# Optimization experiments

Measured on AMD Instinct MI355X. Metric: run time of the kernel, lower is better.

Reference implementation:

```python
import jax, jax.numpy as jnp
import numpy as np

MUL = 32          # multiplicity of 0e and 1o channels
NRAD = 8          # radial basis size
NPATH = 7         # TP instructions

# Orthonormal symmetric-traceless basis for the real l=2 irrep -> Cartesian map
_B = np.zeros((5, 3, 3))
_s2 = 1.0 / np.sqrt(2.0)
_B[0, 0, 1] = _B[0, 1, 0] = _s2                      # xy
_B[1, 1, 2] = _B[1, 2, 1] = _s2                      # yz
_B[2] = np.diag([-1.0, -1.0, 2.0]) / np.sqrt(6.0)    # 2z^2-x^2-y^2
_B[3, 0, 2] = _B[3, 2, 0] = _s2                      # xz
_B[4] = np.diag([1.0, -1.0, 0.0]) / np.sqrt(2.0)     # x^2-y^2
# w3j(1,2,1)[i,M,k], Frobenius-normalized to 1 (e3nn convention)
C121 = jnp.asarray(np.transpose(_B, (1, 0, 2)) / np.sqrt(5.0), jnp.float32)
INV_SQRT3 = float(1.0 / np.sqrt(3.0))   # w3j(1,1,0) / w3j(0,1,1) / w3j(1,0,1)
A0 = float(1.0 / np.sqrt(64.0))         # path weight, l=0 outs: sqrt(1/fan_in), fan_in=2*32
A1 = float(np.sqrt(3.0 / 96.0))         # path weight, l=1 out: sqrt((2l+1)/fan_in), fan_in=3*32


def setup_inputs() -> dict:
    key = jax.random.key(0)
    ks = jax.random.split(key, 9)
    N, E = 4096, 32768
    x = jax.random.normal(ks[0], (N, 4 * MUL), jnp.float32)
    edge_attr = jax.random.normal(ks[1], (E, 9), jnp.float32)
    edge_length = jax.random.uniform(ks[2], (E,), jnp.float32) * 5.0
    edge_src = jax.random.randint(ks[3], (E,), 0, N)
    edge_dst = jax.random.randint(ks[4], (E,), 0, N)
    W_fc1 = jax.random.normal(ks[5], (NRAD, 64), jnp.float32)
    W_fc2 = jax.random.normal(ks[6], (64, NPATH * MUL * MUL), jnp.float32)
    W_sc_s = jax.random.normal(ks[7], (MUL, MUL), jnp.float32)
    W_sc_v = jax.random.normal(ks[8], (MUL, MUL), jnp.float32)
    return dict(x=x, edge_attr=edge_attr, edge_length=edge_length,
                edge_src=edge_src, edge_dst=edge_dst,
                W_fc1=W_fc1, W_fc2=W_fc2, W_sc_s=W_sc_s, W_sc_v=W_sc_v)


def reference(x, edge_attr, edge_length, edge_src, edge_dst, W_fc1, W_fc2, W_sc_s, W_sc_v):
    N = x.shape[0]
    # radial Gaussian basis: centers linspace(0,5,8), sigma = spacing
    centers = jnp.linspace(0.0, 5.0, NRAD)
    sigma = 5.0 / (NRAD - 1)
    d = edge_length[:, None] - centers[None, :]
    radial = jnp.exp(-d * d / (2.0 * sigma * sigma))
    # radial MLP -> per-edge TP weights (e3nn FullyConnectedNet: W/sqrt(fan_in), silu)
    h = jax.nn.silu(radial @ (W_fc1 / jnp.sqrt(jnp.float32(NRAD))))
    w = h @ (W_fc2 / jnp.sqrt(jnp.float32(64)))          # [E, 7168]
    W = w.reshape(-1, NPATH, MUL, MUL)                    # [E,7,u,w]
    # split node features: 32x0e scalars + 32x1o vectors
    s = x[:, :MUL]
    v = x[:, MUL:].reshape(N, MUL, 3)
    sj = s[edge_src]                                      # [E,u]
    vj = v[edge_src]                                      # [E,u,3]
    y0 = edge_attr[:, 0]
    y1 = edge_attr[:, 1:4]
    y2 = edge_attr[:, 4:9]
    # tensor-product paths
    t00 = sj * y0[:, None]                                            # 0e x 0e
    t11 = jnp.einsum('eui,ei->eu', vj, y1) * INV_SQRT3                # 1o x 1o -> 0e
    out_s = (jnp.einsum('eu,euw->ew', t00, W[:, 0]) +
             jnp.einsum('eu,euw->ew', t11, W[:, 1])) * A0             # scalars
    out_g = (jnp.einsum('eu,euw->ew', t00, W[:, 2]) +
             jnp.einsum('eu,euw->ew', t11, W[:, 3])) * A0             # gates
    t01 = sj[:, :, None] * y1[:, None, :] * INV_SQRT3                 # 0e x 1o -> 1o
    t10 = vj * (y0[:, None, None] * INV_SQRT3)                        # 1o x 0e -> 1o
    t12 = jnp.einsum('eui,imk,em->euk', vj, C121, y2)                 # 1o x 2e -> 1o
    out_v = (jnp.einsum('euk,euw->ewk', t01, W[:, 4]) +
             jnp.einsum('euk,euw->ewk', t10, W[:, 5]) +
             jnp.einsum('euk,euw->ewk', t12, W[:, 6])) * A1           # [E,w,3]
    m_ij = jnp.concatenate([out_s, out_g, out_v.reshape(-1, 3 * MUL)], axis=1)  # [E,160]
    # scatter-mean over destination nodes
    sums = jax.ops.segment_sum(m_ij, edge_dst, num_segments=N)
    cnt = jax.ops.segment_sum(jnp.ones((m_ij.shape[0],), m_ij.dtype), edge_dst, num_segments=N)
    m_i = sums / jnp.clip(cnt, 1.0)[:, None]
    # gate: silu on scalars, sigmoid gates multiply the 1o block per-channel
    gs = jax.nn.silu(m_i[:, :MUL])
    gate = jax.nn.sigmoid(m_i[:, MUL:2 * MUL])
    gv = m_i[:, 2 * MUL:].reshape(N, MUL, 3) * gate[:, :, None]
    # residual self-connection (e3nn o3.Linear: per-irrep, / sqrt(mul_in))
    inv_sqrt_mul = 1.0 / jnp.sqrt(jnp.float32(MUL))
    h_s = gs + (s @ W_sc_s) * inv_sqrt_mul
    h_v = gv + jnp.einsum('nui,uw->nwi', v, W_sc_v) * inv_sqrt_mul
    # o3.Norm: per-irrep L2 norm over the (2l+1) components
    norm_s = jnp.sqrt(h_s * h_s + 1e-12)
    norm_v = jnp.sqrt(jnp.sum(h_v * h_v, axis=-1) + 1e-12)
    return jnp.concatenate([norm_s, norm_v], axis=1)       # [N, 64]
```

## Files before the change

kernel.cpp:

```cpp
#include <hip/hip_runtime.h>

#define NIVL  256
#define KINV  51.2f
#define KSTEP 0.01953125f
#define TPW   7168
#define BCAP  256
#define DCAP  64
#define NROW  11
#define TSTR  40
#define TPACK 448

typedef __attribute__((ext_vector_type(8))) __bf16 bf16x8;
typedef __attribute__((ext_vector_type(4))) float f32x4;
union FragU { uint4 u; bf16x8 v; };

__device__ __forceinline__ float sigmoidf_(float v) { return 1.f / (1.f + expf(-v)); }
__device__ __forceinline__ unsigned bf16r_(float x) { return (__float_as_uint(x) + 0x8000u) >> 16; }
__device__ __forceinline__ unsigned pk_(float lo, float hi) { return (bf16r_(hi) << 16) | bf16r_(lo); }

__device__ __forceinline__ f32x4 mfma_(bf16x8 a, bf16x8 b, f32x4 c) {
    return __builtin_amdgcn_mfma_f32_16x16x32_bf16(a, b, c, 0, 0, 0);
}

__global__ __launch_bounds__(256)
void prep_kernel(const float* __restrict__ W1, const float* __restrict__ W2,
                 const float* __restrict__ elen, const int* __restrict__ esrc,
                 const int* __restrict__ edst, const float* __restrict__ ea,
                 uint4* __restrict__ Bpk, int* __restrict__ cntL, int* __restrict__ cntD,
                 float* __restrict__ erec, int* __restrict__ sortedD, int E)
{
    __shared__ float hk_s[5][64];
    __shared__ float Tsl[5][1024];
    const int tid = threadIdx.x;
    const int vb = blockIdx.x;
    if (vb < TPACK) {
        const int bx = vb % 7;
        const int k0 = (vb / 7) * 4;
        for (int idx = tid; idx < 320; idx += 256) {
            int kk = idx >> 6, c = idx & 63;
            float L = (float)(k0 + kk) * KSTEP;
            float d = 0.f;
#pragma unroll
            for (int r = 0; r < 8; ++r) {
                float dd = L - (float)r * (5.f / 7.f);
                d += expf(-dd * dd * 0.98f) * W1[r * 64 + c];
            }
            d *= 0.3535533906f;
            hk_s[kk][c] = d * sigmoidf_(d) * 0.125f;
        }
        __syncthreads();
        float4 acc[5];
#pragma unroll
        for (int q = 0; q < 5; ++q) acc[q] = make_float4(0.f, 0.f, 0.f, 0.f);
        const int pw = bx * 1024 + tid * 4;
#pragma unroll 4
        for (int c = 0; c < 64; ++c) {
            float4 w4 = *(const float4*)(W2 + (size_t)c * TPW + pw);
#pragma unroll
            for (int q = 0; q < 5; ++q) {
                float hv = hk_s[q][c];
                acc[q].x = fmaf(hv, w4.x, acc[q].x);
                acc[q].y = fmaf(hv, w4.y, acc[q].y);
                acc[q].z = fmaf(hv, w4.z, acc[q].z);
                acc[q].w = fmaf(hv, w4.w, acc[q].w);
            }
        }
        __syncthreads();
#pragma unroll
        for (int q = 0; q < 5; ++q)
            *(float4*)&Tsl[q][tid * 4] = acc[q];
        __syncthreads();
        const int lane_s = tid & 63, whs = (tid >> 6) & 1, ih = tid >> 7;
        const int u0p = (lane_s >> 4) * 8, wp = whs * 16 + (lane_s & 15);
#pragma unroll
        for (int t2 = 0; t2 < 2; ++t2) {
            const int jj = k0 + ih + t2 * 2;
            const int kk = jj - k0;
            unsigned ta[4], dd[4];
#pragma unroll
            for (int q = 0; q < 4; ++q) {
                float a0 = Tsl[kk][(u0p + 2 * q) * 32 + wp];
                float a1 = Tsl[kk][(u0p + 2 * q + 1) * 32 + wp];
                float b0 = Tsl[kk + 1][(u0p + 2 * q) * 32 + wp];
                float b1 = Tsl[kk + 1][(u0p + 2 * q + 1) * 32 + wp];
                ta[q] = pk_(a0, a1);
                dd[q] = pk_(b0 - a0, b1 - a1);
            }
            Bpk[((size_t)jj * 28 + bx * 4 + whs) * 64 + lane_s]     = make_uint4(ta[0], ta[1], ta[2], ta[3]);
            Bpk[((size_t)jj * 28 + bx * 4 + 2 + whs) * 64 + lane_s] = make_uint4(dd[0], dd[1], dd[2], dd[3]);
        }
    } else {
        const float I3 = 0.5773502692f, I5 = 0.4472135955f, S2 = 0.7071067812f;
        const float I6 = 0.4082482905f, T6 = 0.8164965809f;
        int e = (vb - TPACK) * 256 + tid;
        if (e < E) {
            float t = elen[e] * KINV;
            int j = (int)t; j = j > 255 ? 255 : j;
            int pos = atomicAdd(&cntL[j], 1);
            if (pos < BCAP) {
                const float* y = ea + (size_t)e * 9;
                float y0 = y[0];
                float a = y[4], b = y[5], c = y[6], d2 = y[7], ee = y[8];
                float4 r0, r1, r2, r3;
                r0.x = t - (float)j;
                r0.y = __int_as_float(esrc[e]);
                r0.z = 0.f;
                r0.w = y0;
                r1.x = y0 * I3;
                r1.y = y[1] * I3; r1.z = y[2] * I3; r1.w = y[3] * I3;
                r2.x = (-c * I6 + ee * S2) * I5;
                r2.y = a * S2 * I5;
                r2.z = d2 * S2 * I5;
                r2.w = (-c * I6 - ee * S2) * I5;
                r3.x = b * S2 * I5;
                r3.y = c * T6 * I5;
                r3.z = 0.f; r3.w = 0.f;
                float4* dst = (float4*)(erec + ((size_t)j * BCAP + pos) * 16);
                dst[0] = r0; dst[1] = r1; dst[2] = r2; dst[3] = r3;
            }
            int slot = j * BCAP + (pos < BCAP ? pos : BCAP - 1);
            int d = edst[e];
            int pd = atomicAdd(&cntD[d], 1);
            if (pd < DCAP) sortedD[d * DCAP + pd] = slot;
        }
    }
}

__global__ __launch_bounds__(256, 2)
void fold_kernel(const float* __restrict__ x, const int* __restrict__ cntL,
                 const float* __restrict__ erec, const uint4* __restrict__ Bpk,
                 float* __restrict__ msg)
{
    const int j = blockIdx.x >> 1, half = blockIdx.x & 1;
    __shared__ __align__(16) unsigned short TB[2 * NROW * 16 * TSTR];
    __shared__ float ECF[32];
    const int tid = threadIdx.x;

    const int cnt = min(cntL[j], BCAP);
    const int nchunk = (cnt + 31) >> 5;
    const int te = tid & 31, sub = tid >> 5;
    const int wv = tid >> 6, lane = tid & 63;
    const int sg = wv >> 1, wh = wv & 1;
    const int col = lane & 15, quad = lane >> 4;

    float4 er0 = {0,0,0,0}, er1 = {0,0,0,0}, er2 = {0,0,0,0}, er3 = {0,0,0,0};
    if (half < nchunk) {
        int ce = min(32, cnt - (half << 5));
        if (te < ce) {
            const float4* rp = (const float4*)(erec + ((size_t)j * BCAP + (half << 5) + te) * 16);
            er0 = rp[0]; er1 = rp[1]; er2 = rp[2]; er3 = rp[3];
        }
    }

    bf16x8 Bt[7][2];
    {
        const uint4* bp = Bpk + (size_t)j * 28 * 64 + lane;
#pragma unroll
        for (int pl = 0; pl < 7; ++pl) {
            FragU fa; fa.u = bp[(pl * 4 + wh) * 64];     Bt[pl][0] = fa.v;
            FragU fd; fd.u = bp[(pl * 4 + 2 + wh) * 64]; Bt[pl][1] = fd.v;
        }
    }

    const float A0 = 0.125f, A1 = 0.1767766953f;

    for (int ci = half; ci < nchunk; ci += 2) {
        const int base = ci << 5;
        const int cntE = min(32, cnt - base);

        const int u0 = sub * 4;
        float s4[4], vvx[12];
        if (te < cntE) {
            int src = __float_as_int(er0.y);
            const float* xp = x + (size_t)src * 128;
            *(float4*)s4 = *(const float4*)(xp + u0);
            *(float4*)(vvx)     = *(const float4*)(xp + 32 + 3 * u0);
            *(float4*)(vvx + 4) = *(const float4*)(xp + 32 + 3 * u0 + 4);
            *(float4*)(vvx + 8) = *(const float4*)(xp + 32 + 3 * u0 + 8);
        }
        float4 nr0 = {0,0,0,0}, nr1 = {0,0,0,0}, nr2 = {0,0,0,0}, nr3 = {0,0,0,0};
        const int cin = ci + 2;
        if (cin < nchunk) {
            int ce2 = min(32, cnt - (cin << 5));
            if (te < ce2) {
                const float4* rp = (const float4*)(erec + ((size_t)j * BCAP + (cin << 5) + te) * 16);
                nr0 = rp[0]; nr1 = rp[1]; nr2 = rp[2]; nr3 = rp[3];
            }
        }

        __syncthreads();

        {
            const int esg = te >> 4, e16 = te & 15;
            float rv[NROW][4];
            if (te < cntE) {
                float y0 = er0.w;
                float y0i = er1.x, y1i0 = er1.y, y1i1 = er1.z, y1i2 = er1.w;
                float M0 = er2.x, M1 = er2.y, M2 = er2.z, M4 = er2.w;
                float M5 = er3.x, M8 = er3.y;
                if (sub == 0) ECF[te] = er0.x;
#pragma unroll
                for (int up = 0; up < 4; ++up) {
                    float s = s4[up];
                    float v0 = vvx[3 * up], v1 = vvx[3 * up + 1], v2 = vvx[3 * up + 2];
                    rv[0][up] = s * y0;
                    rv[1][up] = v0 * y1i0 + v1 * y1i1 + v2 * y1i2;
                    rv[2][up] = s * y1i0;
                    rv[3][up] = s * y1i1;
                    rv[4][up] = s * y1i2;
                    rv[5][up] = v0 * y0i;
                    rv[6][up] = v1 * y0i;
                    rv[7][up] = v2 * y0i;
                    rv[8][up]  = v0 * M0 + v1 * M1 + v2 * M2;
                    rv[9][up]  = v0 * M1 + v1 * M4 + v2 * M5;
                    rv[10][up] = v0 * M2 + v1 * M5 + v2 * M8;
                }
            } else {
#pragma unroll
                for (int r = 0; r < NROW; ++r)
#pragma unroll
                    for (int up = 0; up < 4; ++up) rv[r][up] = 0.f;
            }
#pragma unroll
            for (int r = 0; r < NROW; ++r) {
                unsigned lo = pk_(rv[r][0], rv[r][1]);
                unsigned hi = pk_(rv[r][2], rv[r][3]);
                *(uint2*)&TB[((esg * NROW + r) * 16 + e16) * TSTR + u0] = make_uint2(lo, hi);
            }
        }
        __syncthreads();

        f32x4 cS0 = {0,0,0,0}, cS1 = {0,0,0,0}, cG0 = {0,0,0,0}, cG1 = {0,0,0,0};
        f32x4 cV[3][2];
#pragma unroll
        for (int k = 0; k < 3; ++k) { cV[k][0] = (f32x4){0,0,0,0}; cV[k][1] = (f32x4){0,0,0,0}; }

        #define LOADA(r) ({ FragU fa_; fa_.u = *(const uint4*)&TB[((sg * NROW + (r)) * 16 + col) * TSTR + quad * 8]; fa_.v; })

        bf16x8 a0 = LOADA(0), a1 = LOADA(1);
        cS0 = mfma_(a0, Bt[0][0], cS0); cS0 = mfma_(a1, Bt[1][0], cS0);
        cS1 = mfma_(a0, Bt[0][1], cS1); cS1 = mfma_(a1, Bt[1][1], cS1);
        cG0 = mfma_(a0, Bt[2][0], cG0); cG0 = mfma_(a1, Bt[3][0], cG0);
        cG1 = mfma_(a0, Bt[2][1], cG1); cG1 = mfma_(a1, Bt[3][1], cG1);
#pragma unroll
        for (int k = 0; k < 3; ++k) {
            bf16x8 ak;
            ak = LOADA(2 + k);
            cV[k][0] = mfma_(ak, Bt[4][0], cV[k][0]);
            cV[k][1] = mfma_(ak, Bt[4][1], cV[k][1]);
            ak = LOADA(5 + k);
            cV[k][0] = mfma_(ak, Bt[5][0], cV[k][0]);
            cV[k][1] = mfma_(ak, Bt[5][1], cV[k][1]);
            ak = LOADA(8 + k);
            cV[k][0] = mfma_(ak, Bt[6][0], cV[k][0]);
            cV[k][1] = mfma_(ak, Bt[6][1], cV[k][1]);
        }

        const int w = wh * 16 + col;
        const int sbase = j * BCAP + base;
#pragma unroll
        for (int reg = 0; reg < 4; ++reg) {
            int e = sg * 16 + quad * 4 + reg;
            if (e < cntE) {
                float f = ECF[e];
                float* mp = msg + (size_t)(sbase + e) * 160;
                mp[w]            = (cS0[reg] + f * cS1[reg]) * A0;
                mp[32 + w]       = (cG0[reg] + f * cG1[reg]) * A0;
                mp[64 + 3 * w]     = (cV[0][0][reg] + f * cV[0][1][reg]) * A1;
                mp[64 + 3 * w + 1] = (cV[1][0][reg] + f * cV[1][1][reg]) * A1;
                mp[64 + 3 * w + 2] = (cV[2][0][reg] + f * cV[2][1][reg]) * A1;
            }
        }
        #undef LOADA
        er0 = nr0; er1 = nr1; er2 = nr2; er3 = nr3;
    }
}

__global__ __launch_bounds__(256)
void node_kernel(const float* __restrict__ x, const float* __restrict__ Wss,
                 const float* __restrict__ Wsv, const float* __restrict__ msg,
                 const int* __restrict__ sortedD, const int* __restrict__ cntD,
                 float* __restrict__ out, int N)
{
    __shared__ float ms[8][160];
    const int tid = threadIdx.x;
    const int n0 = blockIdx.x * 8;
    const float IM = 0.1767766953f;

#pragma unroll
    for (int it = 0; it < 5; ++it) {
        int task = tid + it * 256;
        int nl = task / 160;
        int c = task - nl * 160;
        int n = n0 + nl;
        if (n < N) {
            int cd = cntD[n];
            int cc = cd < DCAP ? cd : DCAP;
            const int* sp = sortedD + n * DCAP;
            float s = 0.f;
            for (int i0 = 0; i0 < cc; i0 += 8) {
                int4 ia = *(const int4*)(sp + i0);
                int4 ib = *(const int4*)(sp + i0 + 4);
                int id[8] = { ia.x, ia.y, ia.z, ia.w, ib.x, ib.y, ib.z, ib.w };
                float p[8];
#pragma unroll
                for (int k = 0; k < 8; ++k)
                    p[k] = (i0 + k < cc) ? msg[(size_t)id[k] * 160 + c] : 0.f;
#pragma unroll
                for (int k = 0; k < 8; ++k) s += p[k];
            }
            ms[nl][c] = s / fmaxf((float)cd, 1.f);
        }
    }
    __syncthreads();

#pragma unroll
    for (int it = 0; it < 2; ++it) {
        int task = tid + it * 256;
        int nl = task >> 6, col = task & 63;
        int n = n0 + nl;
        if (n >= N) continue;
        const float* m  = ms[nl];
        const float* xp = x + (size_t)n * 128;
        if (col < 32) {
            int w = col;
            float mval = m[w];
            float gs = mval * sigmoidf_(mval);
            float dot = 0.f;
#pragma unroll 4
            for (int u = 0; u < 32; ++u) dot += xp[u] * Wss[u * 32 + w];
            float hs = gs + dot * IM;
            out[(size_t)n * 64 + w] = sqrtf(hs * hs + 1e-12f);
        } else {
            int w = col - 32;
            float gate = sigmoidf_(m[32 + w]);
            float g0 = m[64 + 3 * w + 0] * gate;
            float g1 = m[64 + 3 * w + 1] * gate;
            float g2 = m[64 + 3 * w + 2] * gate;
            float d0 = 0.f, d1 = 0.f, d2 = 0.f;
#pragma unroll 4
            for (int u = 0; u < 32; ++u) {
                float wvv = Wsv[u * 32 + w];
                d0 += xp[32 + 3 * u + 0] * wvv;
                d1 += xp[32 + 3 * u + 1] * wvv;
                d2 += xp[32 + 3 * u + 2] * wvv;
            }
            float h0 = g0 + d0 * IM, h1 = g1 + d1 * IM, h2 = g2 + d2 * IM;
            out[(size_t)n * 64 + 32 + w] = sqrtf(h0 * h0 + h1 * h1 + h2 * h2 + 1e-12f);
        }
    }
}

extern "C" void kernel_launch(void* const* d_in, const int* in_sizes, int n_in,
                              void* d_out, int out_size, void* d_ws, size_t ws_size,
                              hipStream_t stream)
{
    const float* x    = (const float*)d_in[0];
    const float* ea   = (const float*)d_in[1];
    const float* elen = (const float*)d_in[2];
    const int*   esrc = (const int*)d_in[3];
    const int*   edst = (const int*)d_in[4];
    const float* W1   = (const float*)d_in[5];
    const float* W2   = (const float*)d_in[6];
    const float* Wss  = (const float*)d_in[7];
    const float* Wsv  = (const float*)d_in[8];
    float* out = (float*)d_out;

    const int N = in_sizes[0] / 128;
    const int E = in_sizes[2];

    float* Bpkf   = (float*)d_ws;
    float* msg    = Bpkf + (size_t)256 * 28 * 64 * 4;
    float* erec   = msg + (size_t)256 * BCAP * 160;
    int*   cntL   = (int*)(erec + (size_t)256 * BCAP * 16);
    int*   cntD   = cntL + 256;
    int*   sortedD= cntD + N;
    uint4* Bpk    = (uint4*)Bpkf;

    hipMemsetAsync(cntL, 0, (size_t)(256 + N) * sizeof(int), stream);

    prep_kernel<<<TPACK + (E + 255) / 256, 256, 0, stream>>>(W1, W2, elen, esrc, edst, ea, Bpk, cntL, cntD, erec, sortedD, E);
    fold_kernel<<<NIVL * 2, 256, 0, stream>>>(x, cntL, erec, Bpk, msg);
    node_kernel<<<(N + 7) / 8, 256, 0, stream>>>(x, Wss, Wsv, msg, sortedD, cntD, out, N);
}
```

Measured before the change: 134.1 us.

## Fuse prep, fold and node kernels into one persistent kernel with grid barriers

Merges the three kernels into a single persistent launch of 512 blocks. Phases are separated by software grid-wide barriers built on an atomic counter, and shared memory is reused across phases through a union. Edge preprocessing becomes a grid-stride loop over the remaining 64 blocks instead of 128 extra blocks. The intent is to remove two kernel launch gaps and tail effects, at the cost of depending on all 512 blocks being co-resident (deadlock risk otherwise) and less parallelism in the edge-binning phase.

```diff
diff --git a/kernel.cpp b/kernel.cpp
--- a/kernel.cpp
+++ b/kernel.cpp
@@ -9,6 +9,7 @@
 #define NROW  11
 #define TSTR  40
 #define TPACK 448
+#define GRID  512
 
 typedef __attribute__((ext_vector_type(8))) __bf16 bf16x8;
 typedef __attribute__((ext_vector_type(4))) float f32x4;
@@ -22,17 +23,40 @@
     return __builtin_amdgcn_mfma_f32_16x16x32_bf16(a, b, c, 0, 0, 0);
 }
 
-__global__ __launch_bounds__(256)
-void prep_kernel(const float* __restrict__ W1, const float* __restrict__ W2,
+__device__ __forceinline__ void gbar(int* cnt, int target) {
+    __syncthreads();
+    if (threadIdx.x == 0) {
+        __threadfence();
+        __hip_atomic_fetch_add(cnt, 1, __ATOMIC_RELAXED, __HIP_MEMORY_SCOPE_AGENT);
+        while (__hip_atomic_load(cnt, __ATOMIC_RELAXED, __HIP_MEMORY_SCOPE_AGENT) < target)
+            __builtin_amdgcn_s_sleep(2);
+        __threadfence();
+    }
+    __syncthreads();
+}
+
+union SharedU {
+    struct { float hk[5][64]; float Tsl[5][1024]; } p1;
+    struct { __align__(16) unsigned short TB[2 * NROW * 16 * TSTR];
+             float ECF[32]; } p2;
+    float ms[8][160];
+};
+
+__global__ __launch_bounds__(256, 2)
+void mega_kernel(const float* __restrict__ x, const float* __restrict__ ea,
                  const float* __restrict__ elen, const int* __restrict__ esrc,
-                 const int* __restrict__ edst, const float* __restrict__ ea,
-                 uint4* __restrict__ Bpk, int* __restrict__ cntL, int* __restrict__ cntD,
-                 float* __restrict__ erec, int* __restrict__ sortedD, int E)
+                 const int* __restrict__ edst, const float* __restrict__ W1,
+                 const float* __restrict__ W2, const float* __restrict__ Wss,
+                 const float* __restrict__ Wsv, float* __restrict__ out,
+                 uint4* __restrict__ Bpk, float* __restrict__ msg,
+                 float* __restrict__ erec, int* __restrict__ cntL,
+                 int* __restrict__ cntD, int* __restrict__ sortedD,
+                 int* __restrict__ bar, int N, int E)
 {
-    __shared__ float hk_s[5][64];
-    __shared__ float Tsl[5][1024];
+    __shared__ SharedU sh;
     const int tid = threadIdx.x;
     const int vb = blockIdx.x;
+
     if (vb < TPACK) {
         const int bx = vb % 7;
         const int k0 = (vb / 7) * 4;
@@ -46,7 +70,7 @@
                 d += expf(-dd * dd * 0.98f) * W1[r * 64 + c];
             }
             d *= 0.3535533906f;
-            hk_s[kk][c] = d * sigmoidf_(d) * 0.125f;
+            sh.p1.hk[kk][c] = d * sigmoidf_(d) * 0.125f;
         }
         __syncthreads();
         float4 acc[5];
@@ -58,7 +82,7 @@
             float4 w4 = *(const float4*)(W2 + (size_t)c * TPW + pw);
 #pragma unroll
             for (int q = 0; q < 5; ++q) {
-                float hv = hk_s[q][c];
+                float hv = sh.p1.hk[q][c];
                 acc[q].x = fmaf(hv, w4.x, acc[q].x);
                 acc[q].y = fmaf(hv, w4.y, acc[q].y);
                 acc[q].z = fmaf(hv, w4.z, acc[q].z);
@@ -68,7 +92,7 @@
         __syncthreads();
 #pragma unroll
         for (int q = 0; q < 5; ++q)
-            *(float4*)&Tsl[q][tid * 4] = acc[q];
+            *(float4*)&sh.p1.Tsl[q][tid * 4] = acc[q];
         __syncthreads();
         const int lane_s = tid & 63, whs = (tid >> 6) & 1, ih = tid >> 7;
         const int u0p = (lane_s >> 4) * 8, wp = whs * 16 + (lane_s & 15);
@@ -79,10 +103,10 @@
             unsigned ta[4], dd[4];
 #pragma unroll
             for (int q = 0; q < 4; ++q) {
-                float a0 = Tsl[kk][(u0p + 2 * q) * 32 + wp];
-                float a1 = Tsl[kk][(u0p + 2 * q + 1) * 32 + wp];
-                float b0 = Tsl[kk + 1][(u0p + 2 * q) * 32 + wp];
-                float b1 = Tsl[kk + 1][(u0p + 2 * q + 1) * 32 + wp];
+                float a0 = sh.p1.Tsl[kk][(u0p + 2 * q) * 32 + wp];
+                float a1 = sh.p1.Tsl[kk][(u0p + 2 * q + 1) * 32 + wp];
+                float b0 = sh.p1.Tsl[kk + 1][(u0p + 2 * q) * 32 + wp];
+                float b1 = sh.p1.Tsl[kk + 1][(u0p + 2 * q + 1) * 32 + wp];
                 ta[q] = pk_(a0, a1);
                 dd[q] = pk_(b0 - a0, b1 - a1);
             }
@@ -92,8 +116,7 @@
     } else {
         const float I3 = 0.5773502692f, I5 = 0.4472135955f, S2 = 0.7071067812f;
         const float I6 = 0.4082482905f, T6 = 0.8164965809f;
-        int e = (vb - TPACK) * 256 + tid;
-        if (e < E) {
+        for (int e = (vb - TPACK) * 256 + tid; e < E; e += (GRID - TPACK) * 256) {
             float t = elen[e] * KINV;
             int j = (int)t; j = j > 255 ? 255 : j;
             int pos = atomicAdd(&cntL[j], 1);
@@ -124,229 +147,217 @@
             if (pd < DCAP) sortedD[d * DCAP + pd] = slot;
         }
     }
-}
-
-__global__ __launch_bounds__(256, 2)
-void fold_kernel(const float* __restrict__ x, const int* __restrict__ cntL,
-                 const float* __restrict__ erec, const uint4* __restrict__ Bpk,
-                 float* __restrict__ msg)
-{
-    const int j = blockIdx.x >> 1, half = blockIdx.x & 1;
-    __shared__ __align__(16) unsigned short TB[2 * NROW * 16 * TSTR];
-    __shared__ float ECF[32];
-    const int tid = threadIdx.x;
-
-    const int cnt = min(cntL[j], BCAP);
-    const int nchunk = (cnt + 31) >> 5;
-    const int te = tid & 31, sub = tid >> 5;
-    const int wv = tid >> 6, lane = tid & 63;
-    const int sg = wv >> 1, wh = wv & 1;
-    const int col = lane & 15, quad = lane >> 4;
-
-    float4 er0 = {0,0,0,0}, er1 = {0,0,0,0}, er2 = {0,0,0,0}, er3 = {0,0,0,0};
-    if (half < nchunk) {
-        int ce = min(32, cnt - (half << 5));
-        if (te < ce) {
-            const float4* rp = (const float4*)(erec + ((size_t)j * BCAP + (half << 5) + te) * 16);
-            er0 = rp[0]; er1 = rp[1]; er2 = rp[2]; er3 = rp[3];
+
+    gbar(&bar[0], GRID);
+
+    {
+        const int j = vb >> 1, half = vb & 1;
+        const int cnt = min(cntL[j], BCAP);
+        const int nchunk = (cnt + 31) >> 5;
+        const int te = tid & 31, sub = tid >> 5;
+        const int wv = tid >> 6, lane = tid & 63;
+        const int sg = wv >> 1, wh = wv & 1;
+        const int col = lane & 15, quad = lane >> 4;
+
+        float4 er0 = {0,0,0,0}, er1 = {0,0,0,0}, er2 = {0,0,0,0}, er3 = {0,0,0,0};
+        if (half < nchunk) {
+            int ce = min(32, cnt - (half << 5));
+            if (te < ce) {
+                const float4* rp = (const float4*)(erec + ((size_t)j * BCAP + (half << 5) + te) * 16);
+                er0 = rp[0]; er1 = rp[1]; er2 = rp[2]; er3 = rp[3];
+            }
+        }
+
+        bf16x8 Bt[7][2];
+        {
+            const uint4* bp = Bpk + (size_t)j * 28 * 64 + lane;
+#pragma unroll
+            for (int pl = 0; pl < 7; ++pl) {
+                FragU fa; fa.u = bp[(pl * 4 + wh) * 64];     Bt[pl][0] = fa.v;
+                FragU fd; fd.u = bp[(pl * 4 + 2 + wh) * 64]; Bt[pl][1] = fd.v;
+            }
+        }
+
+        const float A0 = 0.125f, A1 = 0.1767766953f;
+
+        for (int ci = half; ci < nchunk; ci += 2) {
+            const int base = ci << 5;
+            const int cntE = min(32, cnt - base);
+
+            const int u0 = sub * 4;
+            float s4[4], vvx[12];
+            if (te < cntE) {
+                int src = __float_as_int(er0.y);
+                const float* xp = x + (size_t)src * 128;
+                *(float4*)s4 = *(const float4*)(xp + u0);
+                *(float4*)(vvx)     = *(const float4*)(xp + 32 + 3 * u0);
+                *(float4*)(vvx + 4) = *(const float4*)(xp + 32 + 3 * u0 + 4);
+                *(float4*)(vvx + 8) = *(const float4*)(xp + 32 + 3 * u0 + 8);
+            }
+            float4 nr0 = {0,0,0,0}, nr1 = {0,0,0,0}, nr2 = {0,0,0,0}, nr3 = {0,0,0,0};
+            const int cin = ci + 2;
+            if (cin < nchunk) {
+                int ce2 = min(32, cnt - (cin << 5));
+                if (te < ce2) {
+                    const float4* rp = (const float4*)(erec + ((size_t)j * BCAP + (cin << 5) + te) * 16);
+                    nr0 = rp[0]; nr1 = rp[1]; nr2 = rp[2]; nr3 = rp[3];
+                }
+            }
+
+            __syncthreads();
+
+            {
+                const int esg = te >> 4, e16 = te & 15;
+                float rv[NROW][4];
+                if (te < cntE) {
+                    float y0 = er0.w;
+                    float y0i = er1.x, y1i0 = er1.y, y1i1 = er1.z, y1i2 = er1.w;
+                    float M0 = er2.x, M1 = er2.y, M2 = er2.z, M4 = er2.w;
+                    float M5 = er3.x, M8 = er3.y;
+                    if (sub == 0) sh.p2.ECF[te] = er0.x;
+#pragma unroll
+                    for (int up = 0; up < 4; ++up) {
+                        float s = s4[up];
+                        float v0 = vvx[3 * up], v1 = vvx[3 * up + 1], v2 = vvx[3 * up + 2];
+                        rv[0][up] = s * y0;
+                        rv[1][up] = v0 * y1i0 + v1 * y1i1 + v2 * y1i2;
+                        rv[2][up] = s * y1i0;
+                        rv[3][up] = s * y1i1;
+                        rv[4][up] = s * y1i2;
+                        rv[5][up] = v0 * y0i;
+                        rv[6][up] = v1 * y0i;
+                        rv[7][up] = v2 * y0i;
+                        rv[8][up]  = v0 * M0 + v1 * M1 + v2 * M2;
+                        rv[9][up]  = v0 * M1 + v1 * M4 + v2 * M5;
+                        rv[10][up] = v0 * M2 + v1 * M5 + v2 * M8;
+                    }
+                } else {
+#pragma unroll
+                    for (int r = 0; r < NROW; ++r)
+#pragma unroll
+                        for (int up = 0; up < 4; ++up) rv[r][up] = 0.f;
+                }
+#pragma unroll
+                for (int r = 0; r < NROW; ++r) {
+                    unsigned lo = pk_(rv[r][0], rv[r][1]);
+                    unsigned hi = pk_(rv[r][2], rv[r][3]);
+                    *(uint2*)&sh.p2.TB[((esg * NROW + r) * 16 + e16) * TSTR + u0] = make_uint2(lo, hi);
+                }
+            }
+            __syncthreads();
+
+            f32x4 cS0 = {0,0,0,0}, cS1 = {0,0,0,0}, cG0 = {0,0,0,0}, cG1 = {0,0,0,0};
+            f32x4 cV[3][2];
+#pragma unroll
+            for (int k = 0; k < 3; ++k) { cV[k][0] = (f32x4){0,0,0,0}; cV[k][1] = (f32x4){0,0,0,0}; }
+
+            #define LOADA(r) ({ FragU fa_; fa_.u = *(const uint4*)&sh.p2.TB[((sg * NROW + (r)) * 16 + col) * TSTR + quad * 8]; fa_.v; })
+
+            bf16x8 a0 = LOADA(0), a1 = LOADA(1);
+            cS0 = mfma_(a0, Bt[0][0], cS0); cS0 = mfma_(a1, Bt[1][0], cS0);
+            cS1 = mfma_(a0, Bt[0][1], cS1); cS1 = mfma_(a1, Bt[1][1], cS1);
+            cG0 = mfma_(a0, Bt[2][0], cG0); cG0 = mfma_(a1, Bt[3][0], cG0);
+            cG1 = mfma_(a0, Bt[2][1], cG1); cG1 = mfma_(a1, Bt[3][1], cG1);
+#pragma unroll
+            for (int k = 0; k < 3; ++k) {
+                bf16x8 ak;
+                ak = LOADA(2 + k);
+                cV[k][0] = mfma_(ak, Bt[4][0], cV[k][0]);
+                cV[k][1] = mfma_(ak, Bt[4][1], cV[k][1]);
+                ak = LOADA(5 + k);
+                cV[k][0] = mfma_(ak, Bt[5][0], cV[k][0]);
+                cV[k][1] = mfma_(ak, Bt[5][1], cV[k][1]);
+                ak = LOADA(8 + k);
+                cV[k][0] = mfma_(ak, Bt[6][0], cV[k][0]);
+                cV[k][1] = mfma_(ak, Bt[6][1], cV[k][1]);
+            }
+
+            const int w = wh * 16 + col;
+            const int sbase = j * BCAP + base;
+#pragma unroll
+            for (int reg = 0; reg < 4; ++reg) {
+                int e = sg * 16 + quad * 4 + reg;
+                if (e < cntE) {
+                    float f = sh.p2.ECF[e];
+                    float* mp = msg + (size_t)(sbase + e) * 160;
+                    mp[w]            = (cS0[reg] + f * cS1[reg]) * A0;
+                    mp[32 + w]       = (cG0[reg] + f * cG1[reg]) * A0;
+                    mp[64 + 3 * w]     = (cV[0][0][reg] + f * cV[0][1][reg]) * A1;
+                    mp[64 + 3 * w + 1] = (cV[1][0][reg] + f * cV[1][1][reg]) * A1;
+                    mp[64 + 3 * w + 2] = (cV[2][0][reg] + f * cV[2][1][reg]) * A1;
+                }
+            }
+            #undef LOADA
+            er0 = nr0; er1 = nr1; er2 = nr2; er3 = nr3;
         }
     }
 
-    bf16x8 Bt[7][2];
+    gbar(&bar[1], GRID);
+
     {
-        const uint4* bp = Bpk + (size_t)j * 28 * 64 + lane;
-#pragma unroll
-        for (int pl = 0; pl < 7; ++pl) {
-            FragU fa; fa.u = bp[(pl * 4 + wh) * 64];     Bt[pl][0] = fa.v;
-            FragU fd; fd.u = bp[(pl * 4 + 2 + wh) * 64]; Bt[pl][1] = fd.v;
-        }
-    }
-
-    const float A0 = 0.125f, A1 = 0.1767766953f;
-
-    for (int ci = half; ci < nchunk; ci += 2) {
-        const int base = ci << 5;
-        const int cntE = min(32, cnt - base);
-
-        const int u0 = sub * 4;
-        float s4[4], vvx[12];
-        if (te < cntE) {
-            int src = __float_as_int(er0.y);
-            const float* xp = x + (size_t)src * 128;
-            *(float4*)s4 = *(const float4*)(xp + u0);
-            *(float4*)(vvx)     = *(const float4*)(xp + 32 + 3 * u0);
-            *(float4*)(vvx + 4) = *(const float4*)(xp + 32 + 3 * u0 + 4);
-            *(float4*)(vvx + 8) = *(const float4*)(xp + 32 + 3 * u0 + 8);
-        }
-        float4 nr0 = {0,0,0,0}, nr1 = {0,0,0,0}, nr2 = {0,0,0,0}, nr3 = {0,0,0,0};
-        const int cin = ci + 2;
-        if (cin < nchunk) {
-            int ce2 = min(32, cnt - (cin << 5));
-            if (te < ce2) {
-                const float4* rp = (const float4*)(erec + ((size_t)j * BCAP + (cin << 5) + te) * 16);
-                nr0 = rp[0]; nr1 = rp[1]; nr2 = rp[2]; nr3 = rp[3];
-            }
-        }
-
+        const int n0 = vb * 8;
+        const float IM = 0.1767766953f;
+#pragma unroll
+        for (int it = 0; it < 5; ++it) {
+            int task = tid + it * 256;
+            int nl = task / 160;
+            int c = task - nl * 160;
+            int n = n0 + nl;
+            if (n < N) {
+                int cd = cntD[n];
+                int cc = cd < DCAP ? cd : DCAP;
+                const int* sp = sortedD + n * DCAP;
+                float s = 0.f;
+                for (int i0 = 0; i0 < cc; i0 += 8) {
+                    int4 ia = *(const int4*)(sp + i0);
+                    int4 ib = *(const int4*)(sp + i0 + 4);
+                    int id[8] = { ia.x, ia.y, ia.z, ia.w, ib.x, ib.y, ib.z, ib.w };
+                    float p[8];
+#pragma unroll
+                    for (int k = 0; k < 8; ++k)
+                        p[k] = (i0 + k < cc) ? msg[(size_t)id[k] * 160 + c] : 0.f;
+#pragma unroll
+                    for (int k = 0; k < 8; ++k) s += p[k];
+                }
+                sh.ms[nl][c] = s / fmaxf((float)cd, 1.f);
+            }
+        }
         __syncthreads();
 
-        {
-            const int esg = te >> 4, e16 = te & 15;
-            float rv[NROW][4];
-            if (te < cntE) {
-                float y0 = er0.w;
-                float y0i = er1.x, y1i0 = er1.y, y1i1 = er1.z, y1i2 = er1.w;
-                float M0 = er2.x, M1 = er2.y, M2 = er2.z, M4 = er2.w;
-                float M5 = er3.x, M8 = er3.y;
-                if (sub == 0) ECF[te] = er0.x;
-#pragma unroll
-                for (int up = 0; up < 4; ++up) {
-                    float s = s4[up];
-                    float v0 = vvx[3 * up], v1 = vvx[3 * up + 1], v2 = vvx[3 * up + 2];
-                    rv[0][up] = s * y0;
-                    rv[1][up] = v0 * y1i0 + v1 * y1i1 + v2 * y1i2;
-                    rv[2][up] = s * y1i0;
-                    rv[3][up] = s * y1i1;
-                    rv[4][up] = s * y1i2;
-                    rv[5][up] = v0 * y0i;
-                    rv[6][up] = v1 * y0i;
-                    rv[7][up] = v2 * y0i;
-                    rv[8][up]  = v0 * M0 + v1 * M1 + v2 * M2;
-                    rv[9][up]  = v0 * M1 + v1 * M4 + v2 * M5;
-                    rv[10][up] = v0 * M2 + v1 * M5 + v2 * M8;
-                }
+#pragma unroll
+        for (int it = 0; it < 2; ++it) {
+            int task = tid + it * 256;
+            int nl = task >> 6, colp = task & 63;
+            int n = n0 + nl;
+            if (n >= N) continue;
+            const float* m  = sh.ms[nl];
+            const float* xp = x + (size_t)n * 128;
+            if (colp < 32) {
+                int w = colp;
+                float mval = m[w];
+                float gs = mval * sigmoidf_(mval);
+                float dot = 0.f;
+#pragma unroll 4
+                for (int u = 0; u < 32; ++u) dot += xp[u] * Wss[u * 32 + w];
+                float hs = gs + dot * IM;
+                out[(size_t)n * 64 + w] = sqrtf(hs * hs + 1e-12f);
             } else {
-#pragma unroll
-                for (int r = 0; r < NROW; ++r)
-#pragma unroll
-                    for (int up = 0; up < 4; ++up) rv[r][up] = 0.f;
-            }
-#pragma unroll
-            for (int r = 0; r < NROW; ++r) {
-                unsigned lo = pk_(rv[r][0], rv[r][1]);
-                unsigned hi = pk_(rv[r][2], rv[r][3]);
-                *(uint2*)&TB[((esg * NROW + r) * 16 + e16) * TSTR + u0] = make_uint2(lo, hi);
-            }
-        }
-        __syncthreads();
-
-        f32x4 cS0 = {0,0,0,0}, cS1 = {0,0,0,0}, cG0 = {0,0,0,0}, cG1 = {0,0,0,0};
-        f32x4 cV[3][2];
-#pragma unroll
-        for (int k = 0; k < 3; ++k) { cV[k][0] = (f32x4){0,0,0,0}; cV[k][1] = (f32x4){0,0,0,0}; }
-
-        #define LOADA(r) ({ FragU fa_; fa_.u = *(const uint4*)&TB[((sg * NROW + (r)) * 16 + col) * TSTR + quad * 8]; fa_.v; })
-
-        bf16x8 a0 = LOADA(0), a1 = LOADA(1);
-        cS0 = mfma_(a0, Bt[0][0], cS0); cS0 = mfma_(a1, Bt[1][0], cS0);
-        cS1 = mfma_(a0, Bt[0][1], cS1); cS1 = mfma_(a1, Bt[1][1], cS1);
-        cG0 = mfma_(a0, Bt[2][0], cG0); cG0 = mfma_(a1, Bt[3][0], cG0);
-        cG1 = mfma_(a0, Bt[2][1], cG1); cG1 = mfma_(a1, Bt[3][1], cG1);
-#pragma unroll
-        for (int k = 0; k < 3; ++k) {
-            bf16x8 ak;
-            ak = LOADA(2 + k);
-            cV[k][0] = mfma_(ak, Bt[4][0], cV[k][0]);
-            cV[k][1] = mfma_(ak, Bt[4][1], cV[k][1]);
-            ak = LOADA(5 + k);
-            cV[k][0] = mfma_(ak, Bt[5][0], cV[k][0]);
-            cV[k][1] = mfma_(ak, Bt[5][1], cV[k][1]);
-            ak = LOADA(8 + k);
-            cV[k][0] = mfma_(ak, Bt[6][0], cV[k][0]);
-            cV[k][1] = mfma_(ak, Bt[6][1], cV[k][1]);
-        }
-
-        const int w = wh * 16 + col;
-        const int sbase = j * BCAP + base;
-#pragma unroll
-        for (int reg = 0; reg < 4; ++reg) {
-            int e = sg * 16 + quad * 4 + reg;
-            if (e < cntE) {
-                float f = ECF[e];
-                float* mp = msg + (size_t)(sbase + e) * 160;
-                mp[w]            = (cS0[reg] + f * cS1[reg]) * A0;
-                mp[32 + w]       = (cG0[reg] + f * cG1[reg]) * A0;
-                mp[64 + 3 * w]     = (cV[0][0][reg] + f * cV[0][1][reg]) * A1;
-                mp[64 + 3 * w + 1] = (cV[1][0][reg] + f * cV[1][1][reg]) * A1;
-                mp[64 + 3 * w + 2] = (cV[2][0][reg] + f * cV[2][1][reg]) * A1;
-            }
-        }
-        #undef LOADA
-        er0 = nr0; er1 = nr1; er2 = nr2; er3 = nr3;
-    }
-}
-
-__global__ __launch_bounds__(256)
-void node_kernel(const float* __restrict__ x, const float* __restrict__ Wss,
-                 const float* __restrict__ Wsv, const float* __restrict__ msg,
-                 const int* __restrict__ sortedD, const int* __restrict__ cntD,
-                 float* __restrict__ out, int N)
-{
-    __shared__ float ms[8][160];
-    const int tid = threadIdx.x;
-    const int n0 = blockIdx.x * 8;
-    const float IM = 0.1767766953f;
-
-#pragma unroll
-    for (int it = 0; it < 5; ++it) {
-        int task = tid + it * 256;
-        int nl = task / 160;
-        int c = task - nl * 160;
-        int n = n0 + nl;
-        if (n < N) {
-            int cd = cntD[n];
-            int cc = cd < DCAP ? cd : DCAP;
-            const int* sp = sortedD + n * DCAP;
-            float s = 0.f;
-            for (int i0 = 0; i0 < cc; i0 += 8) {
-                int4 ia = *(const int4*)(sp + i0);
-                int4 ib = *(const int4*)(sp + i0 + 4);
-                int id[8] = { ia.x, ia.y, ia.z, ia.w, ib.x, ib.y, ib.z, ib.w };
-                float p[8];
-#pragma unroll
-                for (int k = 0; k < 8; ++k)
-                    p[k] = (i0 + k < cc) ? msg[(size_t)id[k] * 160 + c] : 0.f;
-#pragma unroll
-                for (int k = 0; k < 8; ++k) s += p[k];
-            }
-            ms[nl][c] = s / fmaxf((float)cd, 1.f);
-        }
-    }
-    __syncthreads();
-
-#pragma unroll
-    for (int it = 0; it < 2; ++it) {
-        int task = tid + it * 256;
-        int nl = task >> 6, col = task & 63;
-        int n = n0 + nl;
-        if (n >= N) continue;
-        const float* m  = ms[nl];
-        const float* xp = x + (size_t)n * 128;
-        if (col < 32) {
-            int w = col;
-            float mval = m[w];
-            float gs = mval * sigmoidf_(mval);
-            float dot = 0.f;
+                int w = colp - 32;
+                float gate = sigmoidf_(m[32 + w]);
+                float g0 = m[64 + 3 * w + 0] * gate;
+                float g1 = m[64 + 3 * w + 1] * gate;
+                float g2 = m[64 + 3 * w + 2] * gate;
+                float d0 = 0.f, d1 = 0.f, d2 = 0.f;
 #pragma unroll 4
-            for (int u = 0; u < 32; ++u) dot += xp[u] * Wss[u * 32 + w];
-            float hs = gs + dot * IM;
-            out[(size_t)n * 64 + w] = sqrtf(hs * hs + 1e-12f);
-        } else {
-            int w = col - 32;
-            float gate = sigmoidf_(m[32 + w]);
-            float g0 = m[64 + 3 * w + 0] * gate;
-            float g1 = m[64 + 3 * w + 1] * gate;
-            float g2 = m[64 + 3 * w + 2] * gate;
-            float d0 = 0.f, d1 = 0.f, d2 = 0.f;
-#pragma unroll 4
-            for (int u = 0; u < 32; ++u) {
-                float wvv = Wsv[u * 32 + w];
-                d0 += xp[32 + 3 * u + 0] * wvv;
-                d1 += xp[32 + 3 * u + 1] * wvv;
-                d2 += xp[32 + 3 * u + 2] * wvv;
-            }
-            float h0 = g0 + d0 * IM, h1 = g1 + d1 * IM, h2 = g2 + d2 * IM;
-            out[(size_t)n * 64 + 32 + w] = sqrtf(h0 * h0 + h1 * h1 + h2 * h2 + 1e-12f);
+                for (int u = 0; u < 32; ++u) {
+                    float wvv = Wsv[u * 32 + w];
+                    d0 += xp[32 + 3 * u + 0] * wvv;
+                    d1 += xp[32 + 3 * u + 1] * wvv;
+                    d2 += xp[32 + 3 * u + 2] * wvv;
+                }
+                float h0 = g0 + d0 * IM, h1 = g1 + d1 * IM, h2 = g2 + d2 * IM;
+                out[(size_t)n * 64 + 32 + w] = sqrtf(h0 * h0 + h1 * h1 + h2 * h2 + 1e-12f);
+            }
         }
     }
 }
@@ -374,12 +385,13 @@
     float* erec   = msg + (size_t)256 * BCAP * 160;
     int*   cntL   = (int*)(erec + (size_t)256 * BCAP * 16);
     int*   cntD   = cntL + 256;
-    int*   sortedD= cntD + N;
+    int*   bar    = cntD + N;
+    int*   sortedD= bar + 2;
     uint4* Bpk    = (uint4*)Bpkf;
 
-    hipMemsetAsync(cntL, 0, (size_t)(256 + N) * sizeof(int), stream);
-
-    prep_kernel<<<TPACK + (E + 255) / 256, 256, 0, stream>>>(W1, W2, elen, esrc, edst, ea, Bpk, cntL, cntD, erec, sortedD, E);
-    fold_kernel<<<NIVL * 2, 256, 0, stream>>>(x, cntL, erec, Bpk, msg);
-    node_kernel<<<(N + 7) / 8, 256, 0, stream>>>(x, Wss, Wsv, msg, sortedD, cntD, out, N);
+    hipMemsetAsync(cntL, 0, (size_t)(256 + N + 2) * sizeof(int), stream);
+
+    mega_kernel<<<GRID, 256, 0, stream>>>(x, ea, elen, esrc, edst, W1, W2, Wss, Wsv,
+                                          out, Bpk, msg, erec, cntL, cntD, sortedD,
+                                          bar, N, E);
 }
```

Result: slower. 242.1 us (+80.5%).
